# Kernel optimization log

Measured on AMD Instinct MI355X. Metric: run time of the kernel, lower is better.

Reference implementation:

```python
import jax, jax.numpy as jnp
import numpy as np

K_PER_CLASS = 10
WINDOW = 7
MIN_MASS = 0.05
EPS = 1e-8


def _pool_sum(x, w):
    # sum-pool over last two dims, stride 1, zero padding w//2 (count_include_pad avg = sum / w^2)
    nd = x.ndim
    return jax.lax.reduce_window(
        x, 0.0, jax.lax.add,
        (1,) * (nd - 2) + (w, w),
        (1,) * nd,
        [(0, 0)] * (nd - 2) + [(w // 2, w // 2)] * 2,
    )


def _l2norm(x, axis):
    # matches torch F.normalize(p=2): x / max(||x||, 1e-12)
    return x / jnp.maximum(jnp.linalg.norm(x, axis=axis, keepdims=True), 1e-12)


def setup_inputs() -> dict:
    key = jax.random.key(0)
    k1, k2, k3 = jax.random.split(key, 3)
    feature_map = jax.random.normal(k1, (8, 512, 96, 96), dtype=jnp.float32)
    prototypes = jax.random.normal(k2, (80, 512), dtype=jnp.float32)
    pseudo_mask = jax.random.randint(k3, (8, 96, 96), 0, 9, dtype=jnp.int32)
    return {"feature_map": feature_map, "prototypes": prototypes, "pseudo_mask": pseudo_mask}


def reference(feature_map, prototypes, pseudo_mask):
    B, D, H, W = feature_map.shape
    K = K_PER_CLASS
    C = prototypes.shape[0] // K
    area = WINDOW * WINDOW

    Fn = _l2norm(feature_map, 1)                       # [B,D,H,W]
    Pn = _l2norm(prototypes, 1).reshape(C, K, D)       # [C,K,D]
    sim = jnp.einsum('bdhw,ckd->bckhw', Fn, Pn)        # [B,C,K,H,W]

    omega = (pseudo_mask[:, None] == (jnp.arange(C) + 1)[None, :, None, None]).astype(sim.dtype)  # [B,C,H,W]

    num = _pool_sum(sim * omega[:, :, None], WINDOW) / area   # [B,C,K,H,W]
    den = _pool_sum(omega, WINDOW) / area                      # [B,C,H,W]
    region = num / (den[:, :, None] + EPS)

    a = region.reshape(B, C, K, H * W).transpose(0, 1, 3, 2)   # [B,C,HW,K]
    valid = (den > MIN_MASS).reshape(B, C, H * W)
    V = valid.sum(-1)                                          # [B,C] int
    Vf = jnp.maximum(V, 1).astype(a.dtype)
    vm = valid[..., None].astype(a.dtype)

    mean = (a * vm).sum(2) / Vf[..., None]                     # [B,C,K]
    a_c = (a - mean[:, :, None]) * vm                          # zero out invalid rows
    nrm = jnp.sqrt((a_c * a_c).sum(2))                         # [B,C,K]
    a_n = a_c / (nrm[:, :, None] + EPS)

    gram = jnp.einsum('bcvk,bcvl->bckl', a_n, a_n) / Vf[..., None, None]  # [B,C,K,K]
    off = gram * (1.0 - jnp.eye(K, dtype=gram.dtype))
    loss_c = (off * off).sum((-1, -2)) / (K * (K - 1))         # [B,C]

    active = (omega.sum((-1, -2)) >= 1.0) & (V >= 2)           # mirrors skip conditions
    af = active.astype(loss_c.dtype)
    per_image = (loss_c * af).sum(-1) / jnp.maximum(af.sum(-1), 1.0)
    return per_image.sum() / B
```

## Files before the change

### kernel.cpp

```cpp
#include <hip/hip_runtime.h>
#include <cstdint>
#include <cstddef>

namespace {
constexpr int Bn = 8, Dn = 512, Hn = 96, Wn = 96, HWn = Hn * Wn;
constexpr int Cn = 8, Kn = 10, CKn = Cn * Kn;
constexpr int NPIX = Bn * HWn;
constexpr int NCHUNK = 4, DCH = Dn / NCHUNK;
constexpr int NMOM = 66;
constexpr int RSTRIP = 8;
constexpr int PROW = 96;
constexpr float EPSF = 1e-8f;
constexpr float MINM = 0.05f;

constexpr size_t oPnTp = 0;
constexpr size_t oS    = oPnTp + (size_t)Dn * PROW;
constexpr size_t oPart = oS + (size_t)Bn * Kn * HWn;
constexpr size_t oMom  = oPart + (size_t)NCHUNK * 11 * NPIX;
constexpr size_t oCnt  = oMom + 64 * NMOM;
constexpr size_t oEnd  = oCnt + 64;
}

__device__ __forceinline__ float wred64(float v) {
#pragma unroll
    for (int o = 32; o > 0; o >>= 1) v += __shfl_down(v, o, 64);
    return v;
}

__global__ __launch_bounds__(64) void k_protonorm(const float* __restrict__ P,
                                                  float* __restrict__ PnTp) {
    int ck = blockIdx.x, lane = threadIdx.x;
    const int c = ck / Kn, kk = ck % Kn;
    float v[8]; float ss = 0.f;
#pragma unroll
    for (int j = 0; j < 8; ++j) { v[j] = P[ck * Dn + lane + 64 * j]; ss += v[j] * v[j]; }
    ss = wred64(ss);
    ss = __shfl(ss, 0, 64);
    float inv = 1.0f / fmaxf(sqrtf(ss), 1e-12f);
#pragma unroll
    for (int j = 0; j < 8; ++j)
        PnTp[(size_t)(lane + 64 * j) * PROW + c * 12 + kk] = v[j] * inv;
}

__global__ __launch_bounds__(256) void k_sim(const float* __restrict__ F,
                                             const float* __restrict__ PnTp,
                                             float* __restrict__ part,
                                             const int* __restrict__ mask) {
    __shared__ float pch[64 * PROW];
    const int tid = threadIdx.x;
    const int pix = blockIdx.x * 256 + tid;
    const int chunk = blockIdx.y;
    const int b = pix / HWn, hw = pix % HWn;

    const int m = mask[pix];
    const int cc = m > 0 ? m - 1 : 0;

    float acc[Kn]; float ss = 0.f;
#pragma unroll
    for (int k = 0; k < Kn; ++k) acc[k] = 0.f;

    for (int p = 0; p < DCH / 64; ++p) {
        const int dbase = chunk * DCH + p * 64;
        __syncthreads();
        {
            const float4* src = (const float4*)&PnTp[(size_t)dbase * PROW];
            float4* dst = (float4*)pch;
#pragma unroll
            for (int i = 0; i < 6; ++i)
                dst[tid + 256 * i] = src[tid + 256 * i];
        }
        __syncthreads();
#pragma unroll 4
        for (int dd = 0; dd < 64; ++dd) {
            float f = F[(size_t)(b * Dn + dbase + dd) * HWn + hw];
            ss += f * f;
            const float4* p4 = (const float4*)&pch[dd * PROW + cc * 12];
            float4 pa = p4[0], pb = p4[1];
            float2 pc = *(const float2*)&pch[dd * PROW + cc * 12 + 8];
            acc[0] += f * pa.x; acc[1] += f * pa.y; acc[2] += f * pa.z; acc[3] += f * pa.w;
            acc[4] += f * pb.x; acc[5] += f * pb.y; acc[6] += f * pb.z; acc[7] += f * pb.w;
            acc[8] += f * pc.x; acc[9] += f * pc.y;
        }
    }
#pragma unroll
    for (int k = 0; k < Kn; ++k)
        part[(size_t)(chunk * 11 + k) * NPIX + pix] = acc[k];
    part[(size_t)(chunk * 11 + 10) * NPIX + pix] = ss;
}

__global__ __launch_bounds__(256) void k_simred(const float* __restrict__ part,
                                                const int* __restrict__ mask,
                                                float* __restrict__ S,
                                                int* __restrict__ cnt) {
    __shared__ int hist[Cn];
    const int tid = threadIdx.x;
    const int pix = blockIdx.x * 256 + tid;
    if (tid < Cn) hist[tid] = 0;
    __syncthreads();

    float acc[Kn]; float ss = 0.f;
#pragma unroll
    for (int k = 0; k < Kn; ++k) acc[k] = 0.f;
#pragma unroll
    for (int ch = 0; ch < NCHUNK; ++ch) {
#pragma unroll
        for (int k = 0; k < Kn; ++k)
            acc[k] += part[(size_t)(ch * 11 + k) * NPIX + pix];
        ss += part[(size_t)(ch * 11 + 10) * NPIX + pix];
    }
    float inv = 1.0f / fmaxf(sqrtf(ss), 1e-12f);
    const int b = pix / HWn, hw = pix % HWn;
#pragma unroll
    for (int k = 0; k < Kn; ++k)
        S[(size_t)(b * Kn + k) * HWn + hw] = acc[k] * inv;

    const int m = mask[pix];
    if (m > 0) atomicAdd(&hist[m - 1], 1);
    __syncthreads();
    if (tid < Cn) atomicAdd(&cnt[(pix / HWn) * Cn + tid], hist[tid]);
}

__global__ __launch_bounds__(256) void k_pool(const int* __restrict__ mask,
                                              const float* __restrict__ S,
                                              float* __restrict__ mom) {
    __shared__ float sNum[Kn][14 * 96];
    __shared__ float sDen[14 * 96];
    __shared__ float red[4][NMOM];
    const int bc = blockIdx.x / 12, strip = blockIdx.x % 12;
    const int c = bc & 7, b = bc >> 3;
    const int h0 = strip * RSTRIP;
    const int tid = threadIdx.x;

    for (int item = tid; item < 14 * 24; item += 256) {
        const int r = item / 24, wg = item % 24;
        const int hh = h0 - 3 + r;
        const int w0 = wg * 4;
        float a[Kn][4];
        float dn[4] = {0.f, 0.f, 0.f, 0.f};
#pragma unroll
        for (int k = 0; k < Kn; ++k)
#pragma unroll
            for (int o = 0; o < 4; ++o) a[k][o] = 0.f;

        if (hh >= 0 && hh < Hn) {
            const int rowb = b * HWn + hh * Wn;
            const float* Srow = &S[(size_t)b * Kn * HWn + hh * Wn];
#pragma unroll
            for (int dc = -3; dc <= 6; ++dc) {
                int ww = w0 + dc;
                if (ww < 0 || ww >= Wn) continue;
                const int olo = dc - 3 > 0 ? dc - 3 : 0;
                const int ohi = dc + 3 < 3 ? dc + 3 : 3;
                if (mask[rowb + ww] == c + 1) {
#pragma unroll
                    for (int o = 0; o < 4; ++o)
                        if (o >= olo && o <= ohi) dn[o] += 1.0f;
#pragma unroll
                    for (int k = 0; k < Kn; ++k) {
                        float s = Srow[(size_t)k * HWn + ww];
#pragma unroll
                        for (int o = 0; o < 4; ++o)
                            if (o >= olo && o <= ohi) a[k][o] += s;
                    }
                }
            }
        }
#pragma unroll
        for (int o = 0; o < 4; ++o) {
            sDen[r * 96 + w0 + o] = dn[o];
#pragma unroll
            for (int k = 0; k < Kn; ++k) sNum[k][r * 96 + w0 + o] = a[k][o];
        }
    }
    __syncthreads();

    float mm[NMOM];
#pragma unroll
    for (int i = 0; i < NMOM; ++i) mm[i] = 0.f;

    for (int out = tid; out < RSTRIP * 96; out += 256) {
        const int oh = out / 96, w = out % 96;
        float den = 0.f;
        float n[Kn];
#pragma unroll
        for (int k = 0; k < Kn; ++k) n[k] = 0.f;
#pragma unroll
        for (int dr = 0; dr < 7; ++dr) {
            const int r = oh + dr;
            den += sDen[r * 96 + w];
#pragma unroll
            for (int k = 0; k < Kn; ++k) n[k] += sNum[k][r * 96 + w];
        }
        float dA = den * (1.0f / 49.0f);
        float inv = 1.0f / (dA + EPSF);
        float vm = (dA > MINM) ? 1.0f : 0.0f;
        float rr[Kn];
#pragma unroll
        for (int k = 0; k < Kn; ++k)
            rr[k] = n[k] * (1.0f / 49.0f) * inv * vm;
        mm[0] += vm;
#pragma unroll
        for (int k = 0; k < Kn; ++k) mm[1 + k] += rr[k];
        int p = 11;
#pragma unroll
        for (int k = 0; k < Kn; ++k)
#pragma unroll
            for (int l = 0; l <= k; ++l, ++p) mm[p] += rr[k] * rr[l];
    }

    const int lane = tid & 63, wv = tid >> 6;
#pragma unroll
    for (int i = 0; i < NMOM; ++i) {
        float x = wred64(mm[i]);
        if (lane == 0) red[wv][i] = x;
    }
    __syncthreads();
    for (int i = tid; i < NMOM; i += 256)
        atomicAdd(&mom[bc * NMOM + i],
                  red[0][i] + red[1][i] + red[2][i] + red[3][i]);
}

__global__ __launch_bounds__(64) void k_final(const float* __restrict__ mom,
                                              const int* __restrict__ cnt,
                                              float* __restrict__ out) {
    const int bc = threadIdx.x;
    float mo[NMOM];
#pragma unroll
    for (int i = 0; i < NMOM; ++i) mo[i] = mom[bc * NMOM + i];
    const float V = mo[0];
    const float Vf = fmaxf(V, 1.0f);
    float Sk[Kn];
#pragma unroll
    for (int k = 0; k < Kn; ++k) Sk[k] = mo[1 + k];

    float M[55];
    {
        int p = 0;
#pragma unroll
        for (int k = 0; k < Kn; ++k)
#pragma unroll
            for (int l = 0; l <= k; ++l, ++p)
                M[p] = mo[11 + p] - Sk[k] * Sk[l] / Vf;
    }
    float nrm[Kn];
#pragma unroll
    for (int k = 0; k < Kn; ++k)
        nrm[k] = sqrtf(fmaxf(M[k * (k + 1) / 2 + k], 0.0f));
    float loss = 0.f;
    {
        int p = 0;
#pragma unroll
        for (int k = 0; k < Kn; ++k) {
#pragma unroll
            for (int l = 0; l <= k; ++l, ++p) {
                if (l == k) continue;
                float g = M[p] / ((nrm[k] + EPSF) * (nrm[l] + EPSF)) / Vf;
                loss += 2.0f * g * g;
            }
        }
    }
    loss *= 1.0f / (float)(Kn * (Kn - 1));
    bool act = (cnt[bc] >= 1) && (V >= 2.0f);
    float sl = act ? loss : 0.f;
    float sa = act ? 1.f : 0.f;
#pragma unroll
    for (int o = 4; o > 0; o >>= 1) {
        sl += __shfl_down(sl, o, 8);
        sa += __shfl_down(sa, o, 8);
    }
    __shared__ float pimg[Bn];
    if ((bc & 7) == 0) pimg[bc >> 3] = sl / fmaxf(sa, 1.0f);
    __syncthreads();
    if (bc == 0) {
        float tot = 0.f;
#pragma unroll
        for (int b = 0; b < Bn; ++b) tot += pimg[b];
        out[0] = tot / (float)Bn;
    }
}

extern "C" void kernel_launch(void* const* d_in, const int* in_sizes, int n_in,
                              void* d_out, int out_size, void* d_ws, size_t ws_size,
                              hipStream_t stream) {
    const float* F  = (const float*)d_in[0];
    const float* P  = (const float*)d_in[1];
    const int* mask = (const int*)d_in[2];
    float* ws = (float*)d_ws;
    float* out = (float*)d_out;

    hipMemsetAsync(ws + oMom, 0, (oEnd - oMom) * sizeof(float), stream);

    k_protonorm<<<CKn, 64, 0, stream>>>(P, ws + oPnTp);
    k_sim<<<dim3(NPIX / 256, NCHUNK), 256, 0, stream>>>(F, ws + oPnTp,
                                                        ws + oPart, mask);
    k_simred<<<NPIX / 256, 256, 0, stream>>>(ws + oPart, mask, ws + oS,
                                             (int*)(ws + oCnt));
    k_pool<<<64 * 12, 256, 0, stream>>>(mask, ws + oS, ws + oMom);
    k_final<<<1, 64, 0, stream>>>(ws + oMom, (const int*)(ws + oCnt), out);
}
```

Baseline: 287.0 us.

## Fuse split-D similarity and reduction kernels into one two-group block

The similarity kernel previously split D into four chunks across a grid dimension and wrote partial sums to a workspace. A separate kernel then reduced those partials, normalized, and built the class histogram. Now each 512-thread block covers 256 pixels with two thread groups, each handling half of D. The groups combine their partials through shared memory and write S directly, which removes the partial buffer round trip and one launch. The memset is also folded into the prototype-normalization kernel. The cost is fewer blocks in flight (288 vs 1152) and a longer serial D loop per thread, which could reduce latency hiding.

Measured after the change: 291.7 us. Within noise of the previous version (+1.6%).

```diff
diff --git a/kernel.cpp b/kernel.cpp
--- a/kernel.cpp
+++ b/kernel.cpp
@@ -6,7 +6,6 @@
 constexpr int Bn = 8, Dn = 512, Hn = 96, Wn = 96, HWn = Hn * Wn;
 constexpr int Cn = 8, Kn = 10, CKn = Cn * Kn;
 constexpr int NPIX = Bn * HWn;
-constexpr int NCHUNK = 4, DCH = Dn / NCHUNK;
 constexpr int NMOM = 66;
 constexpr int RSTRIP = 8;
 constexpr int PROW = 96;
@@ -15,10 +14,10 @@
 
 constexpr size_t oPnTp = 0;
 constexpr size_t oS    = oPnTp + (size_t)Dn * PROW;
-constexpr size_t oPart = oS + (size_t)Bn * Kn * HWn;
-constexpr size_t oMom  = oPart + (size_t)NCHUNK * 11 * NPIX;
+constexpr size_t oMom  = oS + (size_t)Bn * Kn * HWn;
 constexpr size_t oCnt  = oMom + 64 * NMOM;
 constexpr size_t oEnd  = oCnt + 64;
+constexpr int ZN = (int)(oEnd - oMom);
 }
 
 __device__ __forceinline__ float wred64(float v) {
@@ -28,8 +27,11 @@
 }
 
 __global__ __launch_bounds__(64) void k_protonorm(const float* __restrict__ P,
-                                                  float* __restrict__ PnTp) {
+                                                  float* __restrict__ PnTp,
+                                                  float* __restrict__ zero) {
     int ck = blockIdx.x, lane = threadIdx.x;
+    if (ck == 0)
+        for (int i = lane; i < ZN; i += 64) zero[i] = 0.f;
     const int c = ck / Kn, kk = ck % Kn;
     float v[8]; float ss = 0.f;
 #pragma unroll
@@ -42,15 +44,21 @@
         PnTp[(size_t)(lane + 64 * j) * PROW + c * 12 + kk] = v[j] * inv;
 }
 
-__global__ __launch_bounds__(256) void k_sim(const float* __restrict__ F,
+__global__ __launch_bounds__(512) void k_sim(const float* __restrict__ F,
                                              const float* __restrict__ PnTp,
-                                             float* __restrict__ part,
-                                             const int* __restrict__ mask) {
+                                             const int* __restrict__ mask,
+                                             float* __restrict__ S,
+                                             int* __restrict__ cnt) {
     __shared__ float pch[64 * PROW];
+    __shared__ float xch[256 * 13];
+    __shared__ int hist[Cn];
     const int tid = threadIdx.x;
-    const int pix = blockIdx.x * 256 + tid;
-    const int chunk = blockIdx.y;
-    const int b = pix / HWn, hw = pix % HWn;
+    const int px = tid & 255;
+    const int g = tid >> 8;
+    const int pix = blockIdx.x * 256 + px;
+    const int b = blockIdx.x / 36;
+    const int hw = pix - b * HWn;
+    if (tid < Cn) hist[tid] = 0;
 
     const int m = mask[pix];
     const int cc = m > 0 ? m - 1 : 0;
@@ -59,65 +67,54 @@
 #pragma unroll
     for (int k = 0; k < Kn; ++k) acc[k] = 0.f;
 
-    for (int p = 0; p < DCH / 64; ++p) {
-        const int dbase = chunk * DCH + p * 64;
+    for (int p = 0; p < 8; ++p) {
         __syncthreads();
         {
-            const float4* src = (const float4*)&PnTp[(size_t)dbase * PROW];
-            float4* dst = (float4*)pch;
-#pragma unroll
-            for (int i = 0; i < 6; ++i)
-                dst[tid + 256 * i] = src[tid + 256 * i];
+            const float4* src4 = (const float4*)PnTp;
+            float4* dst4 = (float4*)pch;
+#pragma unroll
+            for (int it = 0; it < 3; ++it) {
+                int i = tid + 512 * it;
+                int sd = i / 24, col = i - sd * 24;
+                int q = sd >> 5, dd = sd & 31;
+                int gr = q * 256 + p * 32 + dd;
+                dst4[i] = src4[(size_t)gr * 24 + col];
+            }
         }
         __syncthreads();
+        const float* Fp = &F[(size_t)(b * Dn + g * 256 + p * 32) * HWn + hw];
 #pragma unroll 4
-        for (int dd = 0; dd < 64; ++dd) {
-            float f = F[(size_t)(b * Dn + dbase + dd) * HWn + hw];
+        for (int dd = 0; dd < 32; ++dd) {
+            float f = Fp[(size_t)dd * HWn];
             ss += f * f;
-            const float4* p4 = (const float4*)&pch[dd * PROW + cc * 12];
+            const float4* p4 = (const float4*)&pch[(g * 32 + dd) * PROW + cc * 12];
             float4 pa = p4[0], pb = p4[1];
-            float2 pc = *(const float2*)&pch[dd * PROW + cc * 12 + 8];
+            float2 pc = *(const float2*)&pch[(g * 32 + dd) * PROW + cc * 12 + 8];
             acc[0] += f * pa.x; acc[1] += f * pa.y; acc[2] += f * pa.z; acc[3] += f * pa.w;
             acc[4] += f * pb.x; acc[5] += f * pb.y; acc[6] += f * pb.z; acc[7] += f * pb.w;
             acc[8] += f * pc.x; acc[9] += f * pc.y;
         }
     }
-#pragma unroll
-    for (int k = 0; k < Kn; ++k)
-        part[(size_t)(chunk * 11 + k) * NPIX + pix] = acc[k];
-    part[(size_t)(chunk * 11 + 10) * NPIX + pix] = ss;
-}
-
-__global__ __launch_bounds__(256) void k_simred(const float* __restrict__ part,
-                                                const int* __restrict__ mask,
-                                                float* __restrict__ S,
-                                                int* __restrict__ cnt) {
-    __shared__ int hist[Cn];
-    const int tid = threadIdx.x;
-    const int pix = blockIdx.x * 256 + tid;
-    if (tid < Cn) hist[tid] = 0;
-    __syncthreads();
-
-    float acc[Kn]; float ss = 0.f;
-#pragma unroll
-    for (int k = 0; k < Kn; ++k) acc[k] = 0.f;
-#pragma unroll
-    for (int ch = 0; ch < NCHUNK; ++ch) {
-#pragma unroll
-        for (int k = 0; k < Kn; ++k)
-            acc[k] += part[(size_t)(ch * 11 + k) * NPIX + pix];
-        ss += part[(size_t)(ch * 11 + 10) * NPIX + pix];
-    }
-    float inv = 1.0f / fmaxf(sqrtf(ss), 1e-12f);
-    const int b = pix / HWn, hw = pix % HWn;
-#pragma unroll
-    for (int k = 0; k < Kn; ++k)
-        S[(size_t)(b * Kn + k) * HWn + hw] = acc[k] * inv;
-
-    const int m = mask[pix];
-    if (m > 0) atomicAdd(&hist[m - 1], 1);
-    __syncthreads();
-    if (tid < Cn) atomicAdd(&cnt[(pix / HWn) * Cn + tid], hist[tid]);
+    __syncthreads();
+    if (g == 1) {
+#pragma unroll
+        for (int k = 0; k < Kn; ++k) xch[px * 13 + k] = acc[k];
+        xch[px * 13 + 10] = ss;
+    }
+    __syncthreads();
+    if (g == 0) {
+        float tot[Kn];
+#pragma unroll
+        for (int k = 0; k < Kn; ++k) tot[k] = acc[k] + xch[px * 13 + k];
+        float tss = ss + xch[px * 13 + 10];
+        float inv = 1.0f / fmaxf(sqrtf(tss), 1e-12f);
+#pragma unroll
+        for (int k = 0; k < Kn; ++k)
+            S[(size_t)(b * Kn + k) * HWn + hw] = tot[k] * inv;
+        if (m > 0) atomicAdd(&hist[cc], 1);
+    }
+    __syncthreads();
+    if (tid < Cn) atomicAdd(&cnt[b * Cn + tid], hist[tid]);
 }
 
 __global__ __launch_bounds__(256) void k_pool(const int* __restrict__ mask,
@@ -288,13 +285,9 @@
     float* ws = (float*)d_ws;
     float* out = (float*)d_out;
 
-    hipMemsetAsync(ws + oMom, 0, (oEnd - oMom) * sizeof(float), stream);
-
-    k_protonorm<<<CKn, 64, 0, stream>>>(P, ws + oPnTp);
-    k_sim<<<dim3(NPIX / 256, NCHUNK), 256, 0, stream>>>(F, ws + oPnTp,
-                                                        ws + oPart, mask);
-    k_simred<<<NPIX / 256, 256, 0, stream>>>(ws + oPart, mask, ws + oS,
-                                             (int*)(ws + oCnt));
+    k_protonorm<<<CKn, 64, 0, stream>>>(P, ws + oPnTp, ws + oMom);
+    k_sim<<<NPIX / 256, 512, 0, stream>>>(F, ws + oPnTp, mask, ws + oS,
+                                          (int*)(ws + oCnt));
     k_pool<<<64 * 12, 256, 0, stream>>>(mask, ws + oS, ws + oMom);
     k_final<<<1, 64, 0, stream>>>(ws + oMom, (const int*)(ws + oCnt), out);
 }
```
